# Optimization experiments

Measured on AMD Instinct MI355X. Metric: run time of the kernel, lower is better.

Reference implementation:

```python
import jax, jax.numpy as jnp
import numpy as np

B, N, D = 2, 4096, 640      # batch, latent tokens, model dim
H, DH = 8, 80               # heads, head dim (H*DH == D)
CN, CD = 77, 768            # context tokens, context dim (CLIP)
FF = 4 * D                  # GEGLU inner dim = 2560
EPS = 1e-5


def _ln(x, w, b):
    m = jnp.mean(x, axis=-1, keepdims=True)
    v = jnp.mean(jnp.square(x - m), axis=-1, keepdims=True)
    return (x - m) * jax.lax.rsqrt(v + EPS) * w + b


def _attn(xq, xkv, wq, wk, wv, wo, bo):
    b, n, _ = xq.shape
    m = xkv.shape[1]
    q = (xq @ wq).reshape(b, n, H, DH).transpose(0, 2, 1, 3)   # b h n d
    k = (xkv @ wk).reshape(b, m, H, DH).transpose(0, 2, 1, 3)  # b h m d
    v = (xkv @ wv).reshape(b, m, H, DH).transpose(0, 2, 1, 3)
    scores = jnp.einsum('bhid,bhjd->bhij', q, k) * (DH ** -0.5)
    attn = jax.nn.softmax(scores, axis=-1)
    out = jnp.einsum('bhij,bhjd->bhid', attn, v)
    out = out.transpose(0, 2, 1, 3).reshape(b, n, H * DH)
    return out @ wo + bo


def setup_inputs() -> dict:
    key = jax.random.key(0)
    ks = jax.random.split(key, 20)
    s = 0.02
    r = lambda k, sh: (jax.random.normal(k, sh, jnp.float32) * s)
    return {
        'x': jax.random.normal(ks[0], (B, N, D), jnp.float32),
        'context': jax.random.normal(ks[1], (B, CN, CD), jnp.float32),
        'ln1_w': jnp.ones((D,), jnp.float32), 'ln1_b': jnp.zeros((D,), jnp.float32),
        'ln2_w': jnp.ones((D,), jnp.float32), 'ln2_b': jnp.zeros((D,), jnp.float32),
        'ln3_w': jnp.ones((D,), jnp.float32), 'ln3_b': jnp.zeros((D,), jnp.float32),
        'wq1': r(ks[2], (D, D)), 'wk1': r(ks[3], (D, D)), 'wv1': r(ks[4], (D, D)),
        'wo1': r(ks[5], (D, D)), 'bo1': jnp.zeros((D,), jnp.float32),
        'wq2': r(ks[6], (D, D)), 'wk2': r(ks[7], (CD, D)), 'wv2': r(ks[8], (CD, D)),
        'wo2': r(ks[9], (D, D)), 'bo2': jnp.zeros((D,), jnp.float32),
        'w_ff1': r(ks[10], (D, 2 * FF)), 'b_ff1': jnp.zeros((2 * FF,), jnp.float32),
        'w_ff2': r(ks[11], (FF, D)), 'b_ff2': jnp.zeros((D,), jnp.float32),
    }


def reference(x, context,
              ln1_w, ln1_b, ln2_w, ln2_b, ln3_w, ln3_b,
              wq1, wk1, wv1, wo1, bo1,
              wq2, wk2, wv2, wo2, bo2,
              w_ff1, b_ff1, w_ff2, b_ff2):
    # self-attention block
    h = _ln(x, ln1_w, ln1_b)
    x = _attn(h, h, wq1, wk1, wv1, wo1, bo1) + x
    # cross-attention block (k/v from context)
    h = _ln(x, ln2_w, ln2_b)
    x = _attn(h, context, wq2, wk2, wv2, wo2, bo2) + x
    # GEGLU feed-forward
    h = _ln(x, ln3_w, ln3_b)
    proj = h @ w_ff1 + b_ff1
    a, g = jnp.split(proj, 2, axis=-1)
    ff = (a * jax.nn.gelu(g, approximate=False)) @ w_ff2 + b_ff2
    return ff + x
```

## Files before the change

### kernel.cpp

```cpp
#include <hip/hip_runtime.h>
#include <hip/hip_bf16.h>

typedef __hip_bfloat16 bf16;
typedef short s16x8 __attribute__((ext_vector_type(8)));
typedef short s16x4 __attribute__((ext_vector_type(4)));
typedef float f32x4 __attribute__((ext_vector_type(4)));

#define SCALE_DH 0.11180339887498949f
#define QSCALE   0.16129820878f

static __device__ __forceinline__ float b2f(short u) {
  union { float f; unsigned int i; } x;
  x.i = ((unsigned int)(unsigned short)u) << 16;
  return x.f;
}

static __device__ __forceinline__ void gload16(const bf16* g, bf16* l) {
  __builtin_amdgcn_global_load_lds((__attribute__((address_space(1))) const void*)g,
                                   (__attribute__((address_space(3))) void*)l, 16, 0, 0);
}

struct PrepArgs {
  const float* src[10];
  bf16* dst[10];
  int R[10], C[10], cb[10], base[10];
  int cvtbase;
  const float* ctx;
  bf16* ctxb;
};

__global__ __launch_bounds__(256) void prep_kernel(PrepArgs a) {
  const int bid = blockIdx.x;
  if (bid >= a.cvtbase) {
    const int n = 154 * 768;
    int i = ((bid - a.cvtbase) * 256 + threadIdx.x) * 4;
    if (i + 4 <= n) {
      float4 v = *(const float4*)(a.ctx + i);
      a.ctxb[i + 0] = __float2bfloat16(v.x);
      a.ctxb[i + 1] = __float2bfloat16(v.y);
      a.ctxb[i + 2] = __float2bfloat16(v.z);
      a.ctxb[i + 3] = __float2bfloat16(v.w);
    } else {
      for (int k = i; k < n; ++k) a.ctxb[k] = __float2bfloat16(a.ctx[k]);
    }
    return;
  }
  int jid = 0;
#pragma unroll
  for (int k = 1; k < 10; ++k)
    if (bid >= a.base[k]) jid = k;
  const float* in = a.src[jid];
  bf16* out = a.dst[jid];
  const int R = a.R[jid], C = a.C[jid];
  const int lb = bid - a.base[jid];
  const int cblk = lb % a.cb[jid], rblk = lb / a.cb[jid];
  __shared__ float t[32][33];
  const int tx = threadIdx.x & 31, ty = threadIdx.x >> 5;
  const long r0 = (long)rblk * 32, c0 = (long)cblk * 32;
#pragma unroll
  for (int i = 0; i < 4; ++i)
    t[ty + 8 * i][tx] = in[(r0 + ty + 8 * i) * C + c0 + tx];
  __syncthreads();
#pragma unroll
  for (int i = 0; i < 4; ++i)
    out[(c0 + ty + 8 * i) * R + r0 + tx] = __float2bfloat16(t[tx][ty + 8 * i]);
}

__global__ __launch_bounds__(256) void ln_kernel(const float* __restrict__ x,
                                                 const float* __restrict__ w,
                                                 const float* __restrict__ b,
                                                 bf16* __restrict__ out) {
  const int wv = threadIdx.x >> 6, l = threadIdx.x & 63;
  const long row = (long)blockIdx.x * 4 + wv;
  const float* xr = x + row * 640;
  float v[10];
  float s = 0.f;
#pragma unroll
  for (int j = 0; j < 10; ++j) { v[j] = xr[l + 64 * j]; s += v[j]; }
#pragma unroll
  for (int o = 32; o > 0; o >>= 1) s += __shfl_xor(s, o);
  const float mean = s * (1.f / 640.f);
  float vs = 0.f;
#pragma unroll
  for (int j = 0; j < 10; ++j) { float d = v[j] - mean; vs += d * d; }
#pragma unroll
  for (int o = 32; o > 0; o >>= 1) vs += __shfl_xor(vs, o);
  const float rstd = rsqrtf(vs * (1.f / 640.f) + 1e-5f);
  bf16* orow = out + row * 640;
#pragma unroll
  for (int j = 0; j < 10; ++j) {
    int d = l + 64 * j;
    orow[d] = __float2bfloat16((v[j] - mean) * rstd * w[d] + b[d]);
  }
}

template <int EPI>
__global__ __launch_bounds__(256) void gemm_kernel(const bf16* __restrict__ A,
                                                   const bf16* __restrict__ Bt,
                                                   const float* __restrict__ bias,
                                                   const float* __restrict__ res,
                                                   void* __restrict__ Cout,
                                                   int M, int K, int ldc) {
  __shared__ bf16 Ash[128 * 64];
  __shared__ bf16 Bsh[128 * 64];
  const int tid = threadIdx.x, w = tid >> 6, l = tid & 63;
  const int m0 = blockIdx.x * 128, n0 = blockIdx.y * 128;
  const int mb = (w >> 1) * 64, nb = (w & 1) * 64;
  const int lo = l & 15, lg = l >> 4, lo7 = l & 7;
  const f32x4 fz = {0.f, 0.f, 0.f, 0.f};
  f32x4 acc[4][4];
#pragma unroll
  for (int i = 0; i < 4; ++i)
#pragma unroll
    for (int j = 0; j < 4; ++j) acc[i][j] = fz;

  const int g = tid;
  const int gr = g >> 3;
  const int gcsw = 8 * ((g & 7) ^ (gr & 7));
  const bf16* pa[4];
  const bf16* pb[4];
  bf16* la[4];
  bf16* lb[4];
#pragma unroll
  for (int s = 0; s < 4; ++s) {
    const int rl = gr + 32 * s;
    int ra = m0 + rl; if (ra >= M) ra = M - 1;
    pa[s] = A + (long)ra * K + gcsw;
    pb[s] = Bt + (long)(n0 + rl) * K + gcsw;
    la[s] = Ash + (g + 256 * s) * 8;
    lb[s] = Bsh + (g + 256 * s) * 8;
  }

  for (int k0 = 0; k0 < K; k0 += 64) {
    __syncthreads();
#pragma unroll
    for (int s = 0; s < 4; ++s) {
      gload16(pa[s], la[s]); pa[s] += 64;
      gload16(pb[s], lb[s]); pb[s] += 64;
    }
    __syncthreads();
#pragma unroll
    for (int kk = 0; kk < 2; ++kk) {
      const int sl = ((kk * 4 + lg) ^ lo7) * 8;
      s16x8 a[4], b[4];
#pragma unroll
      for (int i = 0; i < 4; ++i)
        a[i] = *(const s16x8*)(Ash + (mb + i * 16 + lo) * 64 + sl);
#pragma unroll
      for (int j = 0; j < 4; ++j)
        b[j] = *(const s16x8*)(Bsh + (nb + j * 16 + lo) * 64 + sl);
#pragma unroll
      for (int i = 0; i < 4; ++i)
#pragma unroll
        for (int j = 0; j < 4; ++j)
          acc[i][j] = __builtin_amdgcn_mfma_f32_16x16x32_bf16(a[i], b[j], acc[i][j], 0, 0, 0);
    }
  }
  const int rb = m0 + mb + lg * 4;
  const int cb = n0 + nb + lo;
#pragma unroll
  for (int i = 0; i < 4; ++i) {
#pragma unroll
    for (int j = 0; j < 4; ++j) {
      const int col = cb + j * 16;
      float bv = 0.f;
      if (EPI == 2) bv = bias[col];
      if (EPI == 3 && col >= 1280) {
        const int t = col - 1280;
        const int hh = t / 80, dh = t % 80;
        const int row0 = rb + i * 16;
        const int bb = row0 >> 12, n = row0 & 4095;
        s16x4 pk;
#pragma unroll
        for (int r = 0; r < 4; ++r)
          pk[r] = (short)__bfloat16_as_ushort(__float2bfloat16(acc[i][j][r]));
        bf16* vt = (bf16*)res;
        *(s16x4*)(vt + (long)(bb * 8 + hh) * 327680 + (long)dh * 4096 + n) = pk;
        continue;
      }
#pragma unroll
      for (int r = 0; r < 4; ++r) {
        const int row = rb + i * 16 + r;
        if (row < M) {
          float v = acc[i][j][r] + bv;
          if (EPI == 2) {
            ((float*)Cout)[(long)row * ldc + col] = v + res[(long)row * ldc + col];
          } else {
            ((bf16*)Cout)[(long)row * ldc + col] = __float2bfloat16(v);
          }
        }
      }
    }
  }
}

template <int EPI>
__global__ __launch_bounds__(256) void gemm64_kernel(const bf16* __restrict__ A,
                                                     const bf16* __restrict__ Bt,
                                                     const float* __restrict__ bias,
                                                     const float* __restrict__ res,
                                                     void* __restrict__ Cout,
                                                     int K, int ldc) {
  __shared__ bf16 Ash[64 * 64];
  __shared__ bf16 Bsh[128 * 64];
  const int tid = threadIdx.x, w = tid >> 6, l = tid & 63;
  const int m0 = blockIdx.x * 64, n0 = blockIdx.y * 128;
  const int mb = (w & 1) * 32, nb = (w >> 1) * 64;
  const int lo = l & 15, lg = l >> 4, lo7 = l & 7;
  const f32x4 fz = {0.f, 0.f, 0.f, 0.f};
  f32x4 acc[2][4];
#pragma unroll
  for (int i = 0; i < 2; ++i)
#pragma unroll
    for (int j = 0; j < 4; ++j) acc[i][j] = fz;

  const int g = tid;
  const int gr = g >> 3;
  const int gcsw = 8 * ((g & 7) ^ (gr & 7));
  const bf16* pa[2];
  const bf16* pb[4];
  bf16* la[2];
  bf16* lb[4];
#pragma unroll
  for (int s = 0; s < 2; ++s) {
    pa[s] = A + (long)(m0 + gr + 32 * s) * K + gcsw;
    la[s] = Ash + (g + 256 * s) * 8;
  }
#pragma unroll
  for (int s = 0; s < 4; ++s) {
    pb[s] = Bt + (long)(n0 + gr + 32 * s) * K + gcsw;
    lb[s] = Bsh + (g + 256 * s) * 8;
  }

  for (int k0 = 0; k0 < K; k0 += 64) {
    __syncthreads();
#pragma unroll
    for (int s = 0; s < 2; ++s) { gload16(pa[s], la[s]); pa[s] += 64; }
#pragma unroll
    for (int s = 0; s < 4; ++s) { gload16(pb[s], lb[s]); pb[s] += 64; }
    __syncthreads();
#pragma unroll
    for (int kk = 0; kk < 2; ++kk) {
      const int sl = ((kk * 4 + lg) ^ lo7) * 8;
      s16x8 a[2], b[4];
#pragma unroll
      for (int i = 0; i < 2; ++i)
        a[i] = *(const s16x8*)(Ash + (mb + i * 16 + lo) * 64 + sl);
#pragma unroll
      for (int j = 0; j < 4; ++j)
        b[j] = *(const s16x8*)(Bsh + (nb + j * 16 + lo) * 64 + sl);
#pragma unroll
      for (int i = 0; i < 2; ++i)
#pragma unroll
        for (int j = 0; j < 4; ++j)
          acc[i][j] = __builtin_amdgcn_mfma_f32_16x16x32_bf16(a[i], b[j], acc[i][j], 0, 0, 0);
    }
  }
  const int rb = m0 + mb + lg * 4;
  const int cb = n0 + nb + lo;
#pragma unroll
  for (int i = 0; i < 2; ++i) {
#pragma unroll
    for (int j = 0; j < 4; ++j) {
      const int col = cb + j * 16;
      float bv = 0.f;
      if (EPI >= 1) bv = bias[col];
#pragma unroll
      for (int r = 0; r < 4; ++r) {
        const int row = rb + i * 16 + r;
        float v = acc[i][j][r] + bv;
        if (EPI == 2) {
          ((float*)Cout)[(long)row * ldc + col] = v + res[(long)row * ldc + col];
        } else {
          ((bf16*)Cout)[(long)row * ldc + col] = __float2bfloat16(v);
        }
      }
    }
  }
}

__global__ __launch_bounds__(256, 3) void flash_kernel(const bf16* __restrict__ qkv,
                                                       const bf16* __restrict__ vT,
                                                       bf16* __restrict__ OP0,
                                                       bf16* __restrict__ OP1,
                                                       float* __restrict__ L) {
  __shared__ bf16 Ksh[64 * 80];
  __shared__ bf16 Vsh[80 * 64];
  const int bh = blockIdx.y, b = bh >> 3, h = bh & 7;
  const int z = blockIdx.z;
  const int tid = threadIdx.x, w = tid >> 6, l = tid & 63;
  const int r0 = blockIdx.x * 128 + w * 32;
  const int lg = l >> 4, lo = l & 15, lo7 = l & 7;
  const s16x8 sz = {0, 0, 0, 0, 0, 0, 0, 0};
  const f32x4 fz = {0.f, 0.f, 0.f, 0.f};

  s16x8 qa[2][3];
#pragma unroll
  for (int gq = 0; gq < 2; ++gq) {
    const bf16* qp = qkv + (long)(b * 4096 + r0 + gq * 16 + lo) * 1920 + h * 80;
    qa[gq][0] = *(const s16x8*)(qp + lg * 8);
    qa[gq][1] = *(const s16x8*)(qp + 32 + lg * 8);
    qa[gq][2] = (lg < 2) ? *(const s16x8*)(qp + 64 + lg * 8) : sz;
#pragma unroll
    for (int f = 0; f < 3; ++f) {
      s16x8 q = qa[gq][f], r;
#pragma unroll
      for (int i = 0; i < 8; ++i)
        r[i] = (short)(__bfloat16_as_ushort(__float2bfloat16(b2f(q[i]) * QSCALE)));
      qa[gq][f] = r;
    }
  }

  const bf16* kp[3];
  const int nbatch = (w < 2) ? 3 : 2;
#pragma unroll
  for (int it = 0; it < 3; ++it) {
    int g = tid + 256 * it;
    int gc = (g < 640) ? g : 0;
    int krow = gc / 10, ksl = gc % 10;
    int ksrc = (ksl < 8) ? (ksl ^ (krow & 7)) : (8 + ((ksl - 8) ^ ((krow >> 2) & 1)));
    kp[it] = qkv + (long)(b * 4096 + z * 2048 + krow) * 1920 + 640 + h * 80 + ksrc * 8;
  }
  const bf16* vp0 = vT + (long)bh * 327680 + (long)(tid >> 3) * 4096 + z * 2048 +
                    (((tid & 7) ^ ((tid >> 3) & 7)) * 8);
  const int soff0 = tid * 8;

  const int voff0 = (((lg >> 1) + 0) ^ lo7) * 8 + 4 * (lg & 1);
  const int voff1 = (((lg >> 1) + 2) ^ lo7) * 8 + 4 * (lg & 1);
  const int voff2 = (((lg >> 1) + 4) ^ lo7) * 8 + 4 * (lg & 1);
  const int voff3 = (((lg >> 1) + 6) ^ lo7) * 8 + 4 * (lg & 1);

  float lrA = 0.f, lrB = 0.f;
  f32x4 oA[5], oB[5];
#pragma unroll
  for (int dt = 0; dt < 5; ++dt) { oA[dt] = fz; oB[dt] = fz; }

#pragma unroll
  for (int it = 0; it < 3; ++it) {
    if (it < nbatch) {
      gload16(kp[it], Ksh + soff0 + 2048 * it); kp[it] += 64 * 1920;
      gload16(vp0 + (long)it * 131072, Vsh + soff0 + 2048 * it);
    }
  }
  __syncthreads();

  for (int kt = 0; kt < 32; ++kt) {
    unsigned paA[8], paB[8];
    f32x4 s0A, s0B, s1A, s1B;
    {
      s16x8 kb0 = *(const s16x8*)(Ksh + lo * 80 + ((lg ^ lo7)) * 8);
      s16x8 kb1 = *(const s16x8*)(Ksh + lo * 80 + (((4 + lg) ^ lo7)) * 8);
      s16x8 kb2 = (lg < 2) ? *(const s16x8*)(Ksh + lo * 80 + 64 + ((lg ^ ((lo >> 2) & 1))) * 8) : sz;
      __builtin_amdgcn_s_setprio(1);
      s0A = __builtin_amdgcn_mfma_f32_16x16x32_bf16(kb0, qa[0][0], fz, 0, 0, 0);
      s0A = __builtin_amdgcn_mfma_f32_16x16x32_bf16(kb1, qa[0][1], s0A, 0, 0, 0);
      s0A = __builtin_amdgcn_mfma_f32_16x16x32_bf16(kb2, qa[0][2], s0A, 0, 0, 0);
      s0B = __builtin_amdgcn_mfma_f32_16x16x32_bf16(kb0, qa[1][0], fz, 0, 0, 0);
      s0B = __builtin_amdgcn_mfma_f32_16x16x32_bf16(kb1, qa[1][1], s0B, 0, 0, 0);
      s0B = __builtin_amdgcn_mfma_f32_16x16x32_bf16(kb2, qa[1][2], s0B, 0, 0, 0);
      __builtin_amdgcn_s_setprio(0);
    }
#pragma unroll
    for (int ntl = 1; ntl <= 4; ++ntl) {
      if (ntl < 4) {
        s16x8 kb0 = *(const s16x8*)(Ksh + (ntl * 16 + lo) * 80 + ((lg ^ lo7)) * 8);
        s16x8 kb1 = *(const s16x8*)(Ksh + (ntl * 16 + lo) * 80 + (((4 + lg) ^ lo7)) * 8);
        s16x8 kb2 = (lg < 2)
                        ? *(const s16x8*)(Ksh + (ntl * 16 + lo) * 80 + 64 + ((lg ^ ((lo >> 2) & 1))) * 8)
                        : sz;
        __builtin_amdgcn_s_setprio(1);
        s1A = __builtin_amdgcn_mfma_f32_16x16x32_bf16(kb0, qa[0][0], fz, 0, 0, 0);
        s1A = __builtin_amdgcn_mfma_f32_16x16x32_bf16(kb1, qa[0][1], s1A, 0, 0, 0);
        s1A = __builtin_amdgcn_mfma_f32_16x16x32_bf16(kb2, qa[0][2], s1A, 0, 0, 0);
        s1B = __builtin_amdgcn_mfma_f32_16x16x32_bf16(kb0, qa[1][0], fz, 0, 0, 0);
        s1B = __builtin_amdgcn_mfma_f32_16x16x32_bf16(kb1, qa[1][1], s1B, 0, 0, 0);
        s1B = __builtin_amdgcn_mfma_f32_16x16x32_bf16(kb2, qa[1][2], s1B, 0, 0, 0);
        __builtin_amdgcn_s_setprio(0);
      }
      {
        const int pidx = ntl - 1;
        float a0 = __builtin_amdgcn_exp2f(s0A[0]);
        float a1 = __builtin_amdgcn_exp2f(s0A[1]);
        float a2 = __builtin_amdgcn_exp2f(s0A[2]);
        float a3 = __builtin_amdgcn_exp2f(s0A[3]);
        lrA += (a0 + a1) + (a2 + a3);
        unsigned u0, u1;
        asm("v_cvt_pk_bf16_f32 %0, %1, %2" : "=v"(u0) : "v"(a0), "v"(a1));
        asm("v_cvt_pk_bf16_f32 %0, %1, %2" : "=v"(u1) : "v"(a2), "v"(a3));
        paA[pidx * 2] = u0;
        paA[pidx * 2 + 1] = u1;
        float b0 = __builtin_amdgcn_exp2f(s0B[0]);
        float b1 = __builtin_amdgcn_exp2f(s0B[1]);
        float b2 = __builtin_amdgcn_exp2f(s0B[2]);
        float b3 = __builtin_amdgcn_exp2f(s0B[3]);
        lrB += (b0 + b1) + (b2 + b3);
        asm("v_cvt_pk_bf16_f32 %0, %1, %2" : "=v"(u0) : "v"(b0), "v"(b1));
        asm("v_cvt_pk_bf16_f32 %0, %1, %2" : "=v"(u1) : "v"(b2), "v"(b3));
        paB[pidx * 2] = u0;
        paB[pidx * 2 + 1] = u1;
      }
      s0A = s1A;
      s0B = s1B;
    }

    typedef unsigned u32x2 __attribute__((ext_vector_type(2)));
    s16x8 frA0, frA1, frB0, frB1;
    {
      u32x2* p;
      p = (u32x2*)&frA0; p[0] = (u32x2){paA[0], paA[1]}; p[1] = (u32x2){paA[2], paA[3]};
      p = (u32x2*)&frA1; p[0] = (u32x2){paA[4], paA[5]}; p[1] = (u32x2){paA[6], paA[7]};
      p = (u32x2*)&frB0; p[0] = (u32x2){paB[0], paB[1]}; p[1] = (u32x2){paB[2], paB[3]};
      p = (u32x2*)&frB1; p[0] = (u32x2){paB[4], paB[5]}; p[1] = (u32x2){paB[6], paB[7]};
    }

    __syncthreads();

    if (kt < 31) {
#pragma unroll
      for (int it = 0; it < 3; ++it) {
        if (it < nbatch) { gload16(kp[it], Ksh + soff0 + 2048 * it); kp[it] += 64 * 1920; }
      }
    }

    __builtin_amdgcn_s_setprio(1);
#pragma unroll
    for (int dt = 0; dt < 5; ++dt) {
      const bf16* vrow = Vsh + (dt * 16 + lo) * 64;
      s16x4 w00 = *(const s16x4*)(vrow + voff0);
      s16x4 w01 = *(const s16x4*)(vrow + voff1);
      s16x4 w10 = *(const s16x4*)(vrow + voff2);
      s16x4 w11 = *(const s16x4*)(vrow + voff3);
      s16x8 vb0 = __builtin_shufflevector(w00, w01, 0, 1, 2, 3, 4, 5, 6, 7);
      s16x8 vb1 = __builtin_shufflevector(w10, w11, 0, 1, 2, 3, 4, 5, 6, 7);
      oA[dt] = __builtin_amdgcn_mfma_f32_16x16x32_bf16(frA0, vb0, oA[dt], 0, 0, 0);
      oA[dt] = __builtin_amdgcn_mfma_f32_16x16x32_bf16(frA1, vb1, oA[dt], 0, 0, 0);
      oB[dt] = __builtin_amdgcn_mfma_f32_16x16x32_bf16(frB0, vb0, oB[dt], 0, 0, 0);
      oB[dt] = __builtin_amdgcn_mfma_f32_16x16x32_bf16(frB1, vb1, oB[dt], 0, 0, 0);
    }
    __builtin_amdgcn_s_setprio(0);

    __syncthreads();

    if (kt < 31) {
#pragma unroll
      for (int it = 0; it < 3; ++it) {
        if (it < nbatch) gload16(vp0 + (long)(kt + 1) * 64 + (long)it * 131072,
                                 Vsh + soff0 + 2048 * it);
      }
    }
  }

  bf16* OPz = (z == 0) ? OP0 : OP1;
  float* Lz = L + (long)z * 65536 + (long)bh * 4096;
  {
    float ssum = lrA;
    ssum += __shfl_xor(ssum, 16);
    ssum += __shfl_xor(ssum, 32);
    if (l < 16) Lz[r0 + l] = ssum;
    bf16* ob = OPz + (long)(b * 4096 + r0 + lg * 4) * 640 + h * 80 + lo;
#pragma unroll
    for (int r = 0; r < 4; ++r)
#pragma unroll
      for (int dt = 0; dt < 5; ++dt)
        ob[(long)r * 640 + dt * 16] = __float2bfloat16(oA[dt][r]);
  }
  {
    float ssum = lrB;
    ssum += __shfl_xor(ssum, 16);
    ssum += __shfl_xor(ssum, 32);
    if (l < 16) Lz[r0 + 16 + l] = ssum;
    bf16* ob = OPz + (long)(b * 4096 + r0 + 16 + lg * 4) * 640 + h * 80 + lo;
#pragma unroll
    for (int r = 0; r < 4; ++r)
#pragma unroll
      for (int dt = 0; dt < 5; ++dt)
        ob[(long)r * 640 + dt * 16] = __float2bfloat16(oB[dt][r]);
  }
}

__global__ __launch_bounds__(256) void comb_kernel(const bf16* __restrict__ OP0,
                                                   const bf16* __restrict__ OP1,
                                                   const float* __restrict__ L,
                                                   bf16* __restrict__ out) {
  const int wv = threadIdx.x >> 6, l = threadIdx.x & 63;
  const int row = blockIdx.x * 4 + wv;
  const int b = row >> 12, n = row & 4095;
  float linv = 0.f;
  if (l < 8) {
    const long li = (long)(b * 8 + l) * 4096 + n;
    linv = 1.f / (L[li] + L[65536 + li]);
  }
  const bf16* p0 = OP0 + (long)row * 640;
  const bf16* p1 = OP1 + (long)row * 640;
  bf16* o = out + (long)row * 640;
#pragma unroll
  for (int t = 0; t < 2; ++t) {
    const int g = (t == 0) ? l : 64 + l;
    if (t == 0 || l < 16) {
      const float inv = __shfl(linv, g / 10);
      s16x8 v0 = *(const s16x8*)(p0 + g * 8);
      s16x8 v1 = *(const s16x8*)(p1 + g * 8);
      s16x8 r;
#pragma unroll
      for (int i = 0; i < 8; ++i)
        r[i] = (short)__bfloat16_as_ushort(__float2bfloat16((b2f(v0[i]) + b2f(v1[i])) * inv));
      *(s16x8*)(o + g * 8) = r;
    }
  }
}

__global__ __launch_bounds__(256) void cross_kernel(const bf16* __restrict__ q2,
                                                    const bf16* __restrict__ kv2,
                                                    bf16* __restrict__ out) {
  __shared__ bf16 Ksh2[80 * 88];
  __shared__ bf16 Vsh2[80 * 88];
  const int bh = blockIdx.y, b = bh >> 3, h = bh & 7;
  const int tid = threadIdx.x, w = tid >> 6, l = tid & 63;
  const int r0 = blockIdx.x * 128 + w * 32;
  const int lg = l >> 4, lo = l & 15;
  const int sb = l & 48;
  const s16x8 sz = {0, 0, 0, 0, 0, 0, 0, 0};
  const f32x4 fz = {0.f, 0.f, 0.f, 0.f};

  s16x8 qa[2][3];
#pragma unroll
  for (int gq = 0; gq < 2; ++gq) {
    const bf16* qp = q2 + (long)(b * 4096 + r0 + gq * 16 + lo) * 640 + h * 80;
    qa[gq][0] = *(const s16x8*)(qp + lg * 8);
    qa[gq][1] = *(const s16x8*)(qp + 32 + lg * 8);
    qa[gq][2] = (lg < 2) ? *(const s16x8*)(qp + 64 + lg * 8) : sz;
#pragma unroll
    for (int f = 0; f < 3; ++f) {
      s16x8 q = qa[gq][f], r;
#pragma unroll
      for (int i = 0; i < 8; ++i)
        r[i] = (short)(__bfloat16_as_ushort(__float2bfloat16(b2f(q[i]) * QSCALE)));
      qa[gq][f] = r;
    }
  }

  for (int c = tid; c < 800; c += 256) {
    int row = c / 10, s = c % 10;
    s16x8 v = sz;
    if (row < 77)
      v = *(const s16x8*)(kv2 + (long)(b * 77 + row) * 1280 + h * 80 + s * 8);
    *(s16x8*)(Ksh2 + row * 88 + s * 8) = v;
  }
  for (int c = tid; c < 770; c += 256) {
    int j = c / 10, d8 = (c % 10) * 8;
    s16x8 v = *(const s16x8*)(kv2 + (long)(b * 77 + j) * 1280 + 640 + h * 80 + d8);
    const short* vs = (const short*)&v;
#pragma unroll
    for (int i = 0; i < 8; ++i) ((short*)Vsh2)[(d8 + i) * 88 + j] = vs[i];
  }
  if (tid < 240) {
    int d = tid / 3, j = 77 + tid % 3;
    ((short*)Vsh2)[d * 88 + j] = 0;
  }
  __syncthreads();

  float lrA = 0.f, lrB = 0.f;
  f32x4 oA[5], oB[5];
#pragma unroll
  for (int dt = 0; dt < 5; ++dt) { oA[dt] = fz; oB[dt] = fz; }

  unsigned paA[10], paB[10];
  f32x4 s0A, s0B, s1A, s1B;
  {
    s16x8 kb0 = *(const s16x8*)(Ksh2 + lo * 88 + lg * 8);
    s16x8 kb1 = *(const s16x8*)(Ksh2 + lo * 88 + 32 + lg * 8);
    s16x8 kb2 = (lg < 2) ? *(const s16x8*)(Ksh2 + lo * 88 + 64 + lg * 8) : sz;
    __builtin_amdgcn_s_setprio(1);
    s0A = __builtin_amdgcn_mfma_f32_16x16x32_bf16(kb0, qa[0][0], fz, 0, 0, 0);
    s0A = __builtin_amdgcn_mfma_f32_16x16x32_bf16(kb1, qa[0][1], s0A, 0, 0, 0);
    s0A = __builtin_amdgcn_mfma_f32_16x16x32_bf16(kb2, qa[0][2], s0A, 0, 0, 0);
    s0B = __builtin_amdgcn_mfma_f32_16x16x32_bf16(kb0, qa[1][0], fz, 0, 0, 0);
    s0B = __builtin_amdgcn_mfma_f32_16x16x32_bf16(kb1, qa[1][1], s0B, 0, 0, 0);
    s0B = __builtin_amdgcn_mfma_f32_16x16x32_bf16(kb2, qa[1][2], s0B, 0, 0, 0);
    __builtin_amdgcn_s_setprio(0);
  }
#pragma unroll
  for (int ntl = 1; ntl <= 5; ++ntl) {
    if (ntl < 5) {
      s16x8 kb0 = *(const s16x8*)(Ksh2 + (ntl * 16 + lo) * 88 + lg * 8);
      s16x8 kb1 = *(const s16x8*)(Ksh2 + (ntl * 16 + lo) * 88 + 32 + lg * 8);
      s16x8 kb2 = (lg < 2) ? *(const s16x8*)(Ksh2 + (ntl * 16 + lo) * 88 + 64 + lg * 8) : sz;
      __builtin_amdgcn_s_setprio(1);
      s1A = __builtin_amdgcn_mfma_f32_16x16x32_bf16(kb0, qa[0][0], fz, 0, 0, 0);
      s1A = __builtin_amdgcn_mfma_f32_16x16x32_bf16(kb1, qa[0][1], s1A, 0, 0, 0);
      s1A = __builtin_amdgcn_mfma_f32_16x16x32_bf16(kb2, qa[0][2], s1A, 0, 0, 0);
      s1B = __builtin_amdgcn_mfma_f32_16x16x32_bf16(kb0, qa[1][0], fz, 0, 0, 0);
      s1B = __builtin_amdgcn_mfma_f32_16x16x32_bf16(kb1, qa[1][1], s1B, 0, 0, 0);
      s1B = __builtin_amdgcn_mfma_f32_16x16x32_bf16(kb2, qa[1][2], s1B, 0, 0, 0);
      __builtin_amdgcn_s_setprio(0);
    }
    {
      const int pidx = ntl - 1;
      float a0 = __builtin_amdgcn_exp2f(s0A[0]);
      float a1 = __builtin_amdgcn_exp2f(s0A[1]);
      float a2 = __builtin_amdgcn_exp2f(s0A[2]);
      float a3 = __builtin_amdgcn_exp2f(s0A[3]);
      float b0 = __builtin_amdgcn_exp2f(s0B[0]);
      float b1 = __builtin_amdgcn_exp2f(s0B[1]);
      float b2 = __builtin_amdgcn_exp2f(s0B[2]);
      float b3 = __builtin_amdgcn_exp2f(s0B[3]);
      if (pidx == 4) {
        if (lg * 4 + 1 >= 13) { a1 = 0.f; b1 = 0.f; }
        if (lg * 4 + 2 >= 13) { a2 = 0.f; b2 = 0.f; }
        if (lg * 4 + 3 >= 13) { a3 = 0.f; b3 = 0.f; }
      }
      lrA += (a0 + a1) + (a2 + a3);
      lrB += (b0 + b1) + (b2 + b3);
      unsigned u0, u1;
      asm("v_cvt_pk_bf16_f32 %0, %1, %2" : "=v"(u0) : "v"(a0), "v"(a1));
      asm("v_cvt_pk_bf16_f32 %0, %1, %2" : "=v"(u1) : "v"(a2), "v"(a3));
      paA[pidx * 2] = u0;
      paA[pidx * 2 + 1] = u1;
      asm("v_cvt_pk_bf16_f32 %0, %1, %2" : "=v"(u0) : "v"(b0), "v"(b1));
      asm("v_cvt_pk_bf16_f32 %0, %1, %2" : "=v"(u1) : "v"(b2), "v"(b3));
      paB[pidx * 2] = u0;
      paB[pidx * 2 + 1] = u1;
    }
    s0A = s1A;
    s0B = s1B;
  }

  typedef unsigned u32x2 __attribute__((ext_vector_type(2)));
  s16x8 frA0, frA1, frA2, frB0, frB1, frB2;
  {
    u32x2* p;
    p = (u32x2*)&frA0; p[0] = (u32x2){paA[0], paA[1]}; p[1] = (u32x2){paA[2], paA[3]};
    p = (u32x2*)&frA1; p[0] = (u32x2){paA[4], paA[5]}; p[1] = (u32x2){paA[6], paA[7]};
    p = (u32x2*)&frA2; p[0] = (u32x2){paA[8], paA[9]}; p[1] = (u32x2){0u, 0u};
    p = (u32x2*)&frB0; p[0] = (u32x2){paB[0], paB[1]}; p[1] = (u32x2){paB[2], paB[3]};
    p = (u32x2*)&frB1; p[0] = (u32x2){paB[4], paB[5]}; p[1] = (u32x2){paB[6], paB[7]};
    p = (u32x2*)&frB2; p[0] = (u32x2){paB[8], paB[9]}; p[1] = (u32x2){0u, 0u};
  }

  __builtin_amdgcn_s_setprio(1);
#pragma unroll
  for (int dt = 0; dt < 5; ++dt) {
    const bf16* vrow = Vsh2 + (dt * 16 + lo) * 88;
    s16x4 w00 = *(const s16x4*)(vrow + 4 * lg);
    s16x4 w01 = *(const s16x4*)(vrow + 16 + 4 * lg);
    s16x4 w10 = *(const s16x4*)(vrow + 32 + 4 * lg);
    s16x4 w11 = *(const s16x4*)(vrow + 48 + 4 * lg);
    s16x4 w20 = *(const s16x4*)(vrow + 64 + 4 * lg);
    s16x8 vb0 = __builtin_shufflevector(w00, w01, 0, 1, 2, 3, 4, 5, 6, 7);
    s16x8 vb1 = __builtin_shufflevector(w10, w11, 0, 1, 2, 3, 4, 5, 6, 7);
    s16x8 vb2 = __builtin_shufflevector(w20, w20, 0, 1, 2, 3, 0, 1, 2, 3);
    oA[dt] = __builtin_amdgcn_mfma_f32_16x16x32_bf16(frA0, vb0, oA[dt], 0, 0, 0);
    oA[dt] = __builtin_amdgcn_mfma_f32_16x16x32_bf16(frA1, vb1, oA[dt], 0, 0, 0);
    oA[dt] = __builtin_amdgcn_mfma_f32_16x16x32_bf16(frA2, vb2, oA[dt], 0, 0, 0);
    oB[dt] = __builtin_amdgcn_mfma_f32_16x16x32_bf16(frB0, vb0, oB[dt], 0, 0, 0);
    oB[dt] = __builtin_amdgcn_mfma_f32_16x16x32_bf16(frB1, vb1, oB[dt], 0, 0, 0);
    oB[dt] = __builtin_amdgcn_mfma_f32_16x16x32_bf16(frB2, vb2, oB[dt], 0, 0, 0);
  }
  __builtin_amdgcn_s_setprio(0);

  {
    float ssum = lrA;
    ssum += __shfl_xor(ssum, 16);
    ssum += __shfl_xor(ssum, 32);
    const float linv = 1.f / ssum;
    float li[4];
#pragma unroll
    for (int r = 0; r < 4; ++r) li[r] = __shfl(linv, sb + lg * 4 + r);
    bf16* ob = out + (long)(b * 4096 + r0 + lg * 4) * 640 + h * 80 + lo;
#pragma unroll
    for (int r = 0; r < 4; ++r)
#pragma unroll
      for (int dt = 0; dt < 5; ++dt)
        ob[(long)r * 640 + dt * 16] = __float2bfloat16(oA[dt][r] * li[r]);
  }
  {
    float ssum = lrB;
    ssum += __shfl_xor(ssum, 16);
    ssum += __shfl_xor(ssum, 32);
    const float linv = 1.f / ssum;
    float li[4];
#pragma unroll
    for (int r = 0; r < 4; ++r) li[r] = __shfl(linv, sb + lg * 4 + r);
    bf16* ob = out + (long)(b * 4096 + r0 + 16 + lg * 4) * 640 + h * 80 + lo;
#pragma unroll
    for (int r = 0; r < 4; ++r)
#pragma unroll
      for (int dt = 0; dt < 5; ++dt)
        ob[(long)r * 640 + dt * 16] = __float2bfloat16(oB[dt][r] * li[r]);
  }
}

__global__ __launch_bounds__(256) void geglu_kernel(const bf16* __restrict__ A,
                                                    const bf16* __restrict__ Bt,
                                                    const float* __restrict__ bias,
                                                    bf16* __restrict__ Cout) {
  __shared__ bf16 Ash[128 * 64];
  __shared__ bf16 Bsh[2][64 * 64];
  const int tid = threadIdx.x, w = tid >> 6, l = tid & 63;
  const int m0 = blockIdx.x * 128, n0 = blockIdx.y * 64;
  const int lo = l & 15, lg = l >> 4, lo7 = l & 7;
  const int mb = w * 32;
  const f32x4 fz = {0.f, 0.f, 0.f, 0.f};
  f32x4 accA[2][4], accG[2][4];
#pragma unroll
  for (int i = 0; i < 2; ++i)
#pragma unroll
    for (int j = 0; j < 4; ++j) { accA[i][j] = fz; accG[i][j] = fz; }

  const int g = tid;
  const int gr = g >> 3;
  const int gcsw = 8 * ((g & 7) ^ (gr & 7));
  const bf16* pa[4];
  const bf16* pb[2][2];
  bf16* la[4];
  bf16* lb[2][2];
#pragma unroll
  for (int s = 0; s < 4; ++s) {
    pa[s] = A + (long)(m0 + gr + 32 * s) * 640 + gcsw;
    la[s] = Ash + (g + 256 * s) * 8;
  }
#pragma unroll
  for (int q = 0; q < 2; ++q)
#pragma unroll
    for (int s = 0; s < 2; ++s) {
      pb[q][s] = Bt + (long)(n0 + q * 2560 + gr + 32 * s) * 640 + gcsw;
      lb[q][s] = Bsh[q] + (g + 256 * s) * 8;
    }

  for (int k0 = 0; k0 < 640; k0 += 64) {
    __syncthreads();
#pragma unroll
    for (int s = 0; s < 4; ++s) { gload16(pa[s], la[s]); pa[s] += 64; }
#pragma unroll
    for (int q = 0; q < 2; ++q)
#pragma unroll
      for (int s = 0; s < 2; ++s) { gload16(pb[q][s], lb[q][s]); pb[q][s] += 64; }
    __syncthreads();
#pragma unroll
    for (int kk = 0; kk < 2; ++kk) {
      const int sl = ((kk * 4 + lg) ^ lo7) * 8;
      s16x8 a[2], ba[4], bg[4];
#pragma unroll
      for (int i = 0; i < 2; ++i)
        a[i] = *(const s16x8*)(Ash + (mb + i * 16 + lo) * 64 + sl);
#pragma unroll
      for (int j = 0; j < 4; ++j) {
        ba[j] = *(const s16x8*)(Bsh[0] + (j * 16 + lo) * 64 + sl);
        bg[j] = *(const s16x8*)(Bsh[1] + (j * 16 + lo) * 64 + sl);
      }
#pragma unroll
      for (int i = 0; i < 2; ++i)
#pragma unroll
        for (int j = 0; j < 4; ++j) {
          accA[i][j] = __builtin_amdgcn_mfma_f32_16x16x32_bf16(a[i], ba[j], accA[i][j], 0, 0, 0);
          accG[i][j] = __builtin_amdgcn_mfma_f32_16x16x32_bf16(a[i], bg[j], accG[i][j], 0, 0, 0);
        }
    }
  }
#pragma unroll
  for (int i = 0; i < 2; ++i) {
#pragma unroll
    for (int j = 0; j < 4; ++j) {
      const int col = n0 + j * 16 + lo;
      const float bA = bias[col];
      const float bG = bias[2560 + col];
#pragma unroll
      for (int r = 0; r < 4; ++r) {
        const long row = m0 + mb + i * 16 + lg * 4 + r;
        const float av = accA[i][j][r] + bA;
        const float gv = accG[i][j][r] + bG;
        const float ge = 0.5f * gv * (1.f + erff(gv * 0.70710678118654752f));
        Cout[row * 2560 + col] = __float2bfloat16(av * ge);
      }
    }
  }
}

extern "C" void kernel_launch(void* const* d_in, const int* in_sizes, int n_in,
                              void* d_out, int out_size, void* d_ws, size_t ws_size,
                              hipStream_t stream) {
  (void)in_sizes; (void)n_in; (void)out_size; (void)ws_size;
  const float* x    = (const float*)d_in[0];
  const float* ctx  = (const float*)d_in[1];
  const float* ln1w = (const float*)d_in[2];
  const float* ln1b = (const float*)d_in[3];
  const float* ln2w = (const float*)d_in[4];
  const float* ln2b = (const float*)d_in[5];
  const float* ln3w = (const float*)d_in[6];
  const float* ln3b = (const float*)d_in[7];
  const float* wq1  = (const float*)d_in[8];
  const float* wk1  = (const float*)d_in[9];
  const float* wv1  = (const float*)d_in[10];
  const float* wo1  = (const float*)d_in[11];
  const float* bo1  = (const float*)d_in[12];
  const float* wq2  = (const float*)d_in[13];
  const float* wk2  = (const float*)d_in[14];
  const float* wv2  = (const float*)d_in[15];
  const float* wo2  = (const float*)d_in[16];
  const float* bo2  = (const float*)d_in[17];
  const float* wff1 = (const float*)d_in[18];
  const float* bff1 = (const float*)d_in[19];
  const float* wff2 = (const float*)d_in[20];
  const float* bff2 = (const float*)d_in[21];

  char* ws = (char*)d_ws;
  bf16* Wqkv1 = (bf16*)(ws + 0);
  bf16* Wo1t  = (bf16*)(ws + 2457600);
  bf16* Wq2t  = (bf16*)(ws + 3276800);
  bf16* Wkv2t = (bf16*)(ws + 4096000);
  bf16* Wo2t  = (bf16*)(ws + 6062080);
  bf16* Wff1t = (bf16*)(ws + 6881280);
  bf16* Wff2t = (bf16*)(ws + 13434880);
  bf16* Ctxb  = (bf16*)(ws + 16711680);
  bf16* Hln   = (bf16*)(ws + 16948224);
  float* X2f  = (float*)(ws + 27433984);
  float* X3f  = (float*)(ws + 48405504);
  bf16* Qkv   = (bf16*)(ws + 69377024);
  bf16* Ffin  = Qkv;
  bf16* Vt    = (bf16*)(ws + 100834304);
  bf16* Ao    = (bf16*)(ws + 111320064);
  bf16* Q2    = (bf16*)(ws + 121805824);
  bf16* Kv2   = (bf16*)(ws + 132291584);
  bf16* OP0   = (bf16*)(ws + 16948224);
  bf16* OP1   = (bf16*)(ws + 37919744);
  float* Lpar = (float*)(ws + 58891264);
  float* Outf = (float*)d_out;

  dim3 blk(256);

  PrepArgs pa;
  const float* srcs[10] = {wq1, wk1, wv1, wo1, wq2, wk2, wv2, wo2, wff1, wff2};
  bf16* dsts[10] = {Wqkv1, Wqkv1 + 640 * 640, Wqkv1 + 2 * 640 * 640, Wo1t, Wq2t,
                    Wkv2t, Wkv2t + 640 * 768, Wo2t, Wff1t, Wff2t};
  int Rs[10] = {640, 640, 640, 640, 640, 768, 768, 640, 640, 2560};
  int Cs[10] = {640, 640, 640, 640, 640, 640, 640, 640, 5120, 640};
  int baseacc = 0;
  for (int j = 0; j < 10; ++j) {
    pa.src[j] = srcs[j];
    pa.dst[j] = dsts[j];
    pa.R[j] = Rs[j];
    pa.C[j] = Cs[j];
    pa.cb[j] = Cs[j] / 32;
    pa.base[j] = baseacc;
    baseacc += (Cs[j] / 32) * (Rs[j] / 32);
  }
  pa.cvtbase = baseacc;
  pa.ctx = ctx;
  pa.ctxb = Ctxb;
  const int prep_blocks = baseacc + 116;
  prep_kernel<<<prep_blocks, blk, 0, stream>>>(pa);

  ln_kernel<<<2048, blk, 0, stream>>>(x, ln1w, ln1b, Hln);
  gemm_kernel<3><<<dim3(64, 15), blk, 0, stream>>>(Hln, Wqkv1, nullptr, (const float*)Vt, Qkv, 8192, 640, 1920);
  flash_kernel<<<dim3(32, 16, 2), blk, 0, stream>>>(Qkv, Vt, OP0, OP1, Lpar);
  comb_kernel<<<2048, blk, 0, stream>>>(OP0, OP1, Lpar, Ao);
  gemm64_kernel<2><<<dim3(128, 5), blk, 0, stream>>>(Ao, Wo1t, bo1, x, X2f, 640, 640);
  ln_kernel<<<2048, blk, 0, stream>>>(X2f, ln2w, ln2b, Hln);
  gemm64_kernel<0><<<dim3(128, 5), blk, 0, stream>>>(Hln, Wq2t, nullptr, nullptr, Q2, 640, 640);
  gemm_kernel<0><<<dim3(2, 10), blk, 0, stream>>>(Ctxb, Wkv2t, nullptr, nullptr, Kv2, 154, 768, 1280);
  cross_kernel<<<dim3(32, 16), blk, 0, stream>>>(Q2, Kv2, Ao);
  gemm64_kernel<2><<<dim3(128, 5), blk, 0, stream>>>(Ao, Wo2t, bo2, X2f, X3f, 640, 640);
  ln_kernel<<<2048, blk, 0, stream>>>(X3f, ln3w, ln3b, Hln);
  geglu_kernel<<<dim3(64, 40), blk, 0, stream>>>(Hln, Wff1t, bff1, Ffin);
  gemm64_kernel<2><<<dim3(128, 5), blk, 0, stream>>>(Ffin, Wff2t, bff2, X3f, Outf, 2560, 640);
}
```

Baseline: 357.8 us.

## Drop split-K flash attention combine pass and store residual stream in bf16

The flash attention kernel no longer splits the key range across two z-blocks. Each block now iterates over all 4096 keys and normalizes its output in place, so the separate combine kernel and its partial-output traffic are removed. The residual stream between blocks (X2, X3) is also stored as bf16 instead of fp32, which halves residual read and write bandwidth in the GEMM epilogues and layernorm inputs. The costs are half as many flash blocks in flight, which may hurt occupancy or parallelism, and reduced precision in the residual accumulation.

```diff
diff --git a/kernel.cpp b/kernel.cpp
--- a/kernel.cpp
+++ b/kernel.cpp
@@ -14,6 +14,9 @@
   x.i = ((unsigned int)(unsigned short)u) << 16;
   return x.f;
 }
+
+static __device__ __forceinline__ float tof(float x) { return x; }
+static __device__ __forceinline__ float tof(bf16 x) { return __bfloat162float(x); }
 
 static __device__ __forceinline__ void gload16(const bf16* g, bf16* l) {
   __builtin_amdgcn_global_load_lds((__attribute__((address_space(1))) const void*)g,
@@ -66,17 +69,18 @@
     out[(c0 + ty + 8 * i) * R + r0 + tx] = __float2bfloat16(t[tx][ty + 8 * i]);
 }
 
-__global__ __launch_bounds__(256) void ln_kernel(const float* __restrict__ x,
+template <typename T>
+__global__ __launch_bounds__(256) void ln_kernel(const T* __restrict__ x,
                                                  const float* __restrict__ w,
                                                  const float* __restrict__ b,
                                                  bf16* __restrict__ out) {
   const int wv = threadIdx.x >> 6, l = threadIdx.x & 63;
   const long row = (long)blockIdx.x * 4 + wv;
-  const float* xr = x + row * 640;
+  const T* xr = x + row * 640;
   float v[10];
   float s = 0.f;
 #pragma unroll
-  for (int j = 0; j < 10; ++j) { v[j] = xr[l + 64 * j]; s += v[j]; }
+  for (int j = 0; j < 10; ++j) { v[j] = tof(xr[l + 64 * j]); s += v[j]; }
 #pragma unroll
   for (int o = 32; o > 0; o >>= 1) s += __shfl_xor(s, o);
   const float mean = s * (1.f / 640.f);
@@ -163,8 +167,6 @@
 #pragma unroll
     for (int j = 0; j < 4; ++j) {
       const int col = cb + j * 16;
-      float bv = 0.f;
-      if (EPI == 2) bv = bias[col];
       if (EPI == 3 && col >= 1280) {
         const int t = col - 1280;
         const int hh = t / 80, dh = t % 80;
@@ -181,14 +183,8 @@
 #pragma unroll
       for (int r = 0; r < 4; ++r) {
         const int row = rb + i * 16 + r;
-        if (row < M) {
-          float v = acc[i][j][r] + bv;
-          if (EPI == 2) {
-            ((float*)Cout)[(long)row * ldc + col] = v + res[(long)row * ldc + col];
-          } else {
-            ((bf16*)Cout)[(long)row * ldc + col] = __float2bfloat16(v);
-          }
-        }
+        if (row < M)
+          ((bf16*)Cout)[(long)row * ldc + col] = __float2bfloat16(acc[i][j][r]);
       }
     }
   }
@@ -198,7 +194,7 @@
 __global__ __launch_bounds__(256) void gemm64_kernel(const bf16* __restrict__ A,
                                                      const bf16* __restrict__ Bt,
                                                      const float* __restrict__ bias,
-                                                     const float* __restrict__ res,
+                                                     const void* __restrict__ res,
                                                      void* __restrict__ Cout,
                                                      int K, int ldc) {
   __shared__ bf16 Ash[64 * 64];
@@ -264,15 +260,23 @@
     for (int j = 0; j < 4; ++j) {
       const int col = cb + j * 16;
       float bv = 0.f;
-      if (EPI >= 1) bv = bias[col];
+      if (EPI >= 4) bv = bias[col];
 #pragma unroll
       for (int r = 0; r < 4; ++r) {
         const int row = rb + i * 16 + r;
+        const long idx = (long)row * ldc + col;
         float v = acc[i][j][r] + bv;
-        if (EPI == 2) {
-          ((float*)Cout)[(long)row * ldc + col] = v + res[(long)row * ldc + col];
+        if (EPI == 4) {
+          v += ((const float*)res)[idx];
+          ((bf16*)Cout)[idx] = __float2bfloat16(v);
+        } else if (EPI == 5) {
+          v += __bfloat162float(((const bf16*)res)[idx]);
+          ((bf16*)Cout)[idx] = __float2bfloat16(v);
+        } else if (EPI == 6) {
+          v += __bfloat162float(((const bf16*)res)[idx]);
+          ((float*)Cout)[idx] = v;
         } else {
-          ((bf16*)Cout)[(long)row * ldc + col] = __float2bfloat16(v);
+          ((bf16*)Cout)[idx] = __float2bfloat16(v);
         }
       }
     }
@@ -281,16 +285,14 @@
 
 __global__ __launch_bounds__(256, 3) void flash_kernel(const bf16* __restrict__ qkv,
                                                        const bf16* __restrict__ vT,
-                                                       bf16* __restrict__ OP0,
-                                                       bf16* __restrict__ OP1,
-                                                       float* __restrict__ L) {
+                                                       bf16* __restrict__ out) {
   __shared__ bf16 Ksh[64 * 80];
   __shared__ bf16 Vsh[80 * 64];
   const int bh = blockIdx.y, b = bh >> 3, h = bh & 7;
-  const int z = blockIdx.z;
   const int tid = threadIdx.x, w = tid >> 6, l = tid & 63;
   const int r0 = blockIdx.x * 128 + w * 32;
   const int lg = l >> 4, lo = l & 15, lo7 = l & 7;
+  const int sb = l & 48;
   const s16x8 sz = {0, 0, 0, 0, 0, 0, 0, 0};
   const f32x4 fz = {0.f, 0.f, 0.f, 0.f};
 
@@ -319,9 +321,9 @@
     int gc = (g < 640) ? g : 0;
     int krow = gc / 10, ksl = gc % 10;
     int ksrc = (ksl < 8) ? (ksl ^ (krow & 7)) : (8 + ((ksl - 8) ^ ((krow >> 2) & 1)));
-    kp[it] = qkv + (long)(b * 4096 + z * 2048 + krow) * 1920 + 640 + h * 80 + ksrc * 8;
-  }
-  const bf16* vp0 = vT + (long)bh * 327680 + (long)(tid >> 3) * 4096 + z * 2048 +
+    kp[it] = qkv + (long)(b * 4096 + krow) * 1920 + 640 + h * 80 + ksrc * 8;
+  }
+  const bf16* vp0 = vT + (long)bh * 327680 + (long)(tid >> 3) * 4096 +
                     (((tid & 7) ^ ((tid >> 3) & 7)) * 8);
   const int soff0 = tid * 8;
 
@@ -344,7 +346,7 @@
   }
   __syncthreads();
 
-  for (int kt = 0; kt < 32; ++kt) {
+  for (int kt = 0; kt < 64; ++kt) {
     unsigned paA[8], paB[8];
     f32x4 s0A, s0B, s1A, s1B;
     {
@@ -415,7 +417,7 @@
 
     __syncthreads();
 
-    if (kt < 31) {
+    if (kt < 63) {
 #pragma unroll
       for (int it = 0; it < 3; ++it) {
         if (it < nbatch) { gload16(kp[it], Ksh + soff0 + 2048 * it); kp[it] += 64 * 1920; }
@@ -441,7 +443,7 @@
 
     __syncthreads();
 
-    if (kt < 31) {
+    if (kt < 63) {
 #pragma unroll
       for (int it = 0; it < 3; ++it) {
         if (it < nbatch) gload16(vp0 + (long)(kt + 1) * 64 + (long)it * 131072,
@@ -450,62 +452,35 @@
     }
   }
 
-  bf16* OPz = (z == 0) ? OP0 : OP1;
-  float* Lz = L + (long)z * 65536 + (long)bh * 4096;
   {
     float ssum = lrA;
     ssum += __shfl_xor(ssum, 16);
     ssum += __shfl_xor(ssum, 32);
-    if (l < 16) Lz[r0 + l] = ssum;
-    bf16* ob = OPz + (long)(b * 4096 + r0 + lg * 4) * 640 + h * 80 + lo;
+    const float linv = 1.f / ssum;
+    float li[4];
+#pragma unroll
+    for (int r = 0; r < 4; ++r) li[r] = __shfl(linv, sb + lg * 4 + r);
+    bf16* ob = out + (long)(b * 4096 + r0 + lg * 4) * 640 + h * 80 + lo;
 #pragma unroll
     for (int r = 0; r < 4; ++r)
 #pragma unroll
       for (int dt = 0; dt < 5; ++dt)
-        ob[(long)r * 640 + dt * 16] = __float2bfloat16(oA[dt][r]);
+        ob[(long)r * 640 + dt * 16] = __float2bfloat16(oA[dt][r] * li[r]);
   }
   {
     float ssum = lrB;
     ssum += __shfl_xor(ssum, 16);
     ssum += __shfl_xor(ssum, 32);
-    if (l < 16) Lz[r0 + 16 + l] = ssum;
-    bf16* ob = OPz + (long)(b * 4096 + r0 + 16 + lg * 4) * 640 + h * 80 + lo;
+    const float linv = 1.f / ssum;
+    float li[4];
+#pragma unroll
+    for (int r = 0; r < 4; ++r) li[r] = __shfl(linv, sb + lg * 4 + r);
+    bf16* ob = out + (long)(b * 4096 + r0 + 16 + lg * 4) * 640 + h * 80 + lo;
 #pragma unroll
     for (int r = 0; r < 4; ++r)
 #pragma unroll
       for (int dt = 0; dt < 5; ++dt)
-        ob[(long)r * 640 + dt * 16] = __float2bfloat16(oB[dt][r]);
-  }
-}
-
-__global__ __launch_bounds__(256) void comb_kernel(const bf16* __restrict__ OP0,
-                                                   const bf16* __restrict__ OP1,
-                                                   const float* __restrict__ L,
-                                                   bf16* __restrict__ out) {
-  const int wv = threadIdx.x >> 6, l = threadIdx.x & 63;
-  const int row = blockIdx.x * 4 + wv;
-  const int b = row >> 12, n = row & 4095;
-  float linv = 0.f;
-  if (l < 8) {
-    const long li = (long)(b * 8 + l) * 4096 + n;
-    linv = 1.f / (L[li] + L[65536 + li]);
-  }
-  const bf16* p0 = OP0 + (long)row * 640;
-  const bf16* p1 = OP1 + (long)row * 640;
-  bf16* o = out + (long)row * 640;
-#pragma unroll
-  for (int t = 0; t < 2; ++t) {
-    const int g = (t == 0) ? l : 64 + l;
-    if (t == 0 || l < 16) {
-      const float inv = __shfl(linv, g / 10);
-      s16x8 v0 = *(const s16x8*)(p0 + g * 8);
-      s16x8 v1 = *(const s16x8*)(p1 + g * 8);
-      s16x8 r;
-#pragma unroll
-      for (int i = 0; i < 8; ++i)
-        r[i] = (short)__bfloat16_as_ushort(__float2bfloat16((b2f(v0[i]) + b2f(v1[i])) * inv));
-      *(s16x8*)(o + g * 8) = r;
-    }
+        ob[(long)r * 640 + dt * 16] = __float2bfloat16(oB[dt][r] * li[r]);
   }
 }
 
@@ -813,17 +788,14 @@
   bf16* Wff2t = (bf16*)(ws + 13434880);
   bf16* Ctxb  = (bf16*)(ws + 16711680);
   bf16* Hln   = (bf16*)(ws + 16948224);
-  float* X2f  = (float*)(ws + 27433984);
-  float* X3f  = (float*)(ws + 48405504);
+  bf16* X2b   = (bf16*)(ws + 27433984);
+  bf16* X3b   = (bf16*)(ws + 48405504);
   bf16* Qkv   = (bf16*)(ws + 69377024);
   bf16* Ffin  = Qkv;
   bf16* Vt    = (bf16*)(ws + 100834304);
   bf16* Ao    = (bf16*)(ws + 111320064);
   bf16* Q2    = (bf16*)(ws + 121805824);
   bf16* Kv2   = (bf16*)(ws + 132291584);
-  bf16* OP0   = (bf16*)(ws + 16948224);
-  bf16* OP1   = (bf16*)(ws + 37919744);
-  float* Lpar = (float*)(ws + 58891264);
   float* Outf = (float*)d_out;
 
   dim3 blk(256);
@@ -850,17 +822,16 @@
   const int prep_blocks = baseacc + 116;
   prep_kernel<<<prep_blocks, blk, 0, stream>>>(pa);
 
-  ln_kernel<<<2048, blk, 0, stream>>>(x, ln1w, ln1b, Hln);
+  ln_kernel<float><<<2048, blk, 0, stream>>>(x, ln1w, ln1b, Hln);
   gemm_kernel<3><<<dim3(64, 15), blk, 0, stream>>>(Hln, Wqkv1, nullptr, (const float*)Vt, Qkv, 8192, 640, 1920);
-  flash_kernel<<<dim3(32, 16, 2), blk, 0, stream>>>(Qkv, Vt, OP0, OP1, Lpar);
-  comb_kernel<<<2048, blk, 0, stream>>>(OP0, OP1, Lpar, Ao);
-  gemm64_kernel<2><<<dim3(128, 5), blk, 0, stream>>>(Ao, Wo1t, bo1, x, X2f, 640, 640);
-  ln_kernel<<<2048, blk, 0, stream>>>(X2f, ln2w, ln2b, Hln);
+  flash_kernel<<<dim3(32, 16), blk, 0, stream>>>(Qkv, Vt, Ao);
+  gemm64_kernel<4><<<dim3(128, 5), blk, 0, stream>>>(Ao, Wo1t, bo1, x, X2b, 640, 640);
+  ln_kernel<bf16><<<2048, blk, 0, stream>>>(X2b, ln2w, ln2b, Hln);
   gemm64_kernel<0><<<dim3(128, 5), blk, 0, stream>>>(Hln, Wq2t, nullptr, nullptr, Q2, 640, 640);
   gemm_kernel<0><<<dim3(2, 10), blk, 0, stream>>>(Ctxb, Wkv2t, nullptr, nullptr, Kv2, 154, 768, 1280);
   cross_kernel<<<dim3(32, 16), blk, 0, stream>>>(Q2, Kv2, Ao);
-  gemm64_kernel<2><<<dim3(128, 5), blk, 0, stream>>>(Ao, Wo2t, bo2, X2f, X3f, 640, 640);
-  ln_kernel<<<2048, blk, 0, stream>>>(X3f, ln3w, ln3b, Hln);
+  gemm64_kernel<5><<<dim3(128, 5), blk, 0, stream>>>(Ao, Wo2t, bo2, X2b, X3b, 640, 640);
+  ln_kernel<bf16><<<2048, blk, 0, stream>>>(X3b, ln3w, ln3b, Hln);
   geglu_kernel<<<dim3(64, 40), blk, 0, stream>>>(Hln, Wff1t, bff1, Ffin);
-  gemm64_kernel<2><<<dim3(128, 5), blk, 0, stream>>>(Ffin, Wff2t, bff2, X3f, Outf, 2560, 640);
-}
+  gemm64_kernel<6><<<dim3(128, 5), blk, 0, stream>>>(Ffin, Wff2t, bff2, X3b, Outf, 2560, 640);
+}
```

Measured after the change: 345.0 us, median of 2. 1.04x faster.
